# Kernel tuning notes

Measured on AMD Instinct MI355X. Metric: run time of the kernel, lower is better.

Reference implementation:

```python
import jax, jax.numpy as jnp
import numpy as np

B, D, T, C = 128, 128, 2048, 64


def setup_inputs() -> dict:
    key = jax.random.key(0)
    k1, k2, k3 = jax.random.split(key, 3)
    feature = jax.random.normal(k1, (B, D, T), dtype=jnp.float32)
    label = jax.random.randint(k2, (B, T), 0, C, dtype=jnp.int64)
    centers = jax.random.normal(k3, (C, D), dtype=jnp.float32)
    return {"feature": feature, "label": label, "centers": centers}


def reference(feature, label, centers):
    # feature: [B, D, T] -> flatten to [N, D] with N = B*T (transpose(2,1).reshape)
    num_classes, feat_dim = centers.shape
    feat = jnp.transpose(feature, (0, 2, 1)).reshape(-1, feat_dim)  # [N, D]
    lab = label.reshape(-1)                                          # [N]

    centers_batch = centers[lab]                                     # gather [N, D]
    center_loss = jnp.mean((feat - centers_batch) ** 2)              # MSELoss (mean)

    diff = centers_batch - feat                                      # [N, D]
    # scatter-sum of per-row diffs into their class slot (replaces python loop)
    difference = jax.ops.segment_sum(diff, lab, num_segments=num_classes)  # [C, D]
    appear_times = jnp.bincount(lab, length=num_classes)             # [C]
    difference = difference / jnp.clip(appear_times, 1, None).astype(difference.dtype)[:, None]
    return (center_loss, difference)
```

## Files before the change

kernel.cpp:

```cpp
#include <hip/hip_runtime.h>


#define NT 2048
#define NC 64

#define OFF_P     0
#define OFF_SSP   1048576
#define OFF_CNTP  1048832
#define OFF_CROSS 1057024
#define OFF_CC    1057056
#define OFF_SS    1057088

#define WAIT_VM0()   __builtin_amdgcn_s_waitcnt(0x0F70)
#define WAIT_VM4()   __builtin_amdgcn_s_waitcnt(0x0F74)
#define WAIT_LGKM0() __builtin_amdgcn_s_waitcnt(0xC07F)
#define CFENCE()     __asm__ volatile("" ::: "memory")
#define BAR()        do { CFENCE(); __builtin_amdgcn_s_barrier(); CFENCE(); } while (0)

__device__ __forceinline__ void dma16(const float* g, float* l) {
    __builtin_amdgcn_global_load_lds(
        (const __attribute__((address_space(1))) void*)g,
        (__attribute__((address_space(3))) void*)l, 16, 0, 0);
}

__global__ __launch_bounds__(256) void k_main(const float* __restrict__ feat,
                                              const int*  __restrict__ label,
                                              float* __restrict__ ws) {
    __shared__ float rowbuf[2][2][2052];
    __shared__ unsigned short __attribute__((aligned(16))) sorted[4096];
    __shared__ float S_lds[64][33];
    __shared__ float partial[2][256];
    __shared__ int cnt[NC], pstart[NC], ntc[NC], cursor[NC];

    const int tid = threadIdx.x, bid = blockIdx.x;
    const int dh = bid & 1, b = bid >> 1;
    const int wave = tid >> 6, lane = tid & 63;

    for (int j = tid; j < 4096; j += 256) sorted[j] = (unsigned short)8192;
    if (tid < NC) { cnt[tid] = 0; cursor[tid] = 0; }
    if (tid < 4) rowbuf[tid >> 1][tid & 1][2048] = 0.0f;
    __syncthreads();

    const int* lp = label + b * NT + tid * 8;
    const int4 La = *(const int4*)lp;
    const int4 Lb = *(const int4*)(lp + 4);
    atomicAdd(&cnt[La.x], 1); atomicAdd(&cnt[La.y], 1);
    atomicAdd(&cnt[La.z], 1); atomicAdd(&cnt[La.w], 1);
    atomicAdd(&cnt[Lb.x], 1); atomicAdd(&cnt[Lb.y], 1);
    atomicAdd(&cnt[Lb.z], 1); atomicAdd(&cnt[Lb.w], 1);
    __syncthreads();

    if (tid == 0) {
        int pt = 0;
        for (int c = 0; c < NC; ++c) {
            int pl = (cnt[c] + 15) & ~15;
            pstart[c] = pt; ntc[c] = pl >> 4; pt += pl;
        }
    }
    __syncthreads();

    if (dh == 0 && tid < NC) ((int*)(ws + OFF_CNTP))[b * NC + tid] = cnt[tid];

    {
        const int t0 = tid * 8;
        int l, p;
        l = La.x; p = pstart[l] + atomicAdd(&cursor[l], 1); sorted[p] = (unsigned short)((t0 + 0) * 4);
        l = La.y; p = pstart[l] + atomicAdd(&cursor[l], 1); sorted[p] = (unsigned short)((t0 + 1) * 4);
        l = La.z; p = pstart[l] + atomicAdd(&cursor[l], 1); sorted[p] = (unsigned short)((t0 + 2) * 4);
        l = La.w; p = pstart[l] + atomicAdd(&cursor[l], 1); sorted[p] = (unsigned short)((t0 + 3) * 4);
        l = Lb.x; p = pstart[l] + atomicAdd(&cursor[l], 1); sorted[p] = (unsigned short)((t0 + 4) * 4);
        l = Lb.y; p = pstart[l] + atomicAdd(&cursor[l], 1); sorted[p] = (unsigned short)((t0 + 5) * 4);
        l = Lb.z; p = pstart[l] + atomicAdd(&cursor[l], 1); sorted[p] = (unsigned short)((t0 + 6) * 4);
        l = Lb.w; p = pstart[l] + atomicAdd(&cursor[l], 1); sorted[p] = (unsigned short)((t0 + 7) * 4);
    }
    __syncthreads();

    int off[16];
    {
        const uint4 pk0 = *(const uint4*)&sorted[tid * 16];
        const uint4 pk1 = *(const uint4*)&sorted[tid * 16 + 8];
        off[0]  = pk0.x & 0xFFFF; off[1]  = pk0.x >> 16;
        off[2]  = pk0.y & 0xFFFF; off[3]  = pk0.y >> 16;
        off[4]  = pk0.z & 0xFFFF; off[5]  = pk0.z >> 16;
        off[6]  = pk0.w & 0xFFFF; off[7]  = pk0.w >> 16;
        off[8]  = pk1.x & 0xFFFF; off[9]  = pk1.x >> 16;
        off[10] = pk1.y & 0xFFFF; off[11] = pk1.y >> 16;
        off[12] = pk1.z & 0xFFFF; off[13] = pk1.z >> 16;
        off[14] = pk1.w & 0xFFFF; off[15] = pk1.w >> 16;
    }

    const float* fbase = feat + ((size_t)b * 128 + dh * 64) * NT;
    float ss = 0.0f;

    {
        #pragma unroll
        for (int q = 0; q < 4; ++q) {
            int m = wave + 4 * q, r = m >> 3, p = m & 7;
            dma16(fbase + (size_t)r * NT + p * 256 + lane * 4, &rowbuf[0][r][p * 256]);
        }
    }

    for (int i = 0; i < 32; ++i) {
        const int buf = i & 1;
        if (i < 31) {
            const float* base = fbase + (size_t)(2 * (i + 1)) * NT;
            #pragma unroll
            for (int q = 0; q < 4; ++q) {
                int m = wave + 4 * q, r = m >> 3, p = m & 7;
                dma16(base + (size_t)r * NT + p * 256 + lane * 4, &rowbuf[buf ^ 1][r][p * 256]);
            }
            WAIT_VM4();
        } else {
            WAIT_VM0();
        }
        BAR();

        #pragma unroll
        for (int r = 0; r < 2; ++r) {
            const char* rb = (const char*)&rowbuf[buf][r][0];
            float s = 0.0f;
            #pragma unroll
            for (int j = 0; j < 16; ++j) {
                float v = *(const float*)(rb + off[j]);
                s += v; ss += v * v;
            }
            partial[r][tid] = s;
        }
        WAIT_LGKM0();
        BAR();

        if (tid < 128) {
            const int c = tid & 63, r = tid >> 6;
            const int ft = pstart[c] >> 4, n = ntc[c];
            float s = 0.0f;
            for (int j = 0; j < n; ++j) s += partial[r][ft + j];
            S_lds[c][(2 * i + r) & 31] = s;
        }

        if ((i & 15) == 15) {
            WAIT_LGKM0();
            BAR();
            const int dbase = (i >> 4) << 5;
            const int c = tid >> 2, dj0 = (tid & 3) * 8;
            float4 v0, v1;
            v0.x = S_lds[c][dj0 + 0]; v0.y = S_lds[c][dj0 + 1];
            v0.z = S_lds[c][dj0 + 2]; v0.w = S_lds[c][dj0 + 3];
            v1.x = S_lds[c][dj0 + 4]; v1.y = S_lds[c][dj0 + 5];
            v1.z = S_lds[c][dj0 + 6]; v1.w = S_lds[c][dj0 + 7];
            float* dst = ws + OFF_P + (size_t)bid * 4096 + c * 64 + dbase + dj0;
            *(float4*)dst = v0;
            *(float4*)(dst + 4) = v1;
        }
    }

    __syncthreads();
    partial[0][tid] = ss;
    __syncthreads();
    for (int s = 128; s > 0; s >>= 1) {
        if (tid < s) partial[0][tid] += partial[0][tid + s];
        __syncthreads();
    }
    if (tid == 0) ws[OFF_SSP + bid] = partial[0][0];
}

__global__ __launch_bounds__(256) void k_red(float* __restrict__ ws,
                                             const float* __restrict__ centers,
                                             float* __restrict__ out) {
    const int tid = threadIdx.x, bid = blockIdx.x;

    if (bid == 32) {
        __shared__ float r[256];
        r[tid] = ws[OFF_SSP + tid];
        __syncthreads();
        for (int k = 128; k > 0; k >>= 1) { if (tid < k) r[tid] += r[tid + k]; __syncthreads(); }
        if (tid == 0) ws[OFF_SS] = r[0];
        return;
    }

    __shared__ int cred[256];
    __shared__ int cnt[NC];
    {
        const int c = tid & 63, part = tid >> 6;
        const int* cntP = (const int*)(ws + OFF_CNTP);
        int s = 0;
        for (int bb = part * 32; bb < part * 32 + 32; ++bb) s += cntP[bb * NC + c];
        cred[tid] = s;
    }
    __syncthreads();
    if (tid < NC) cnt[tid] = cred[tid] + cred[tid + 64] + cred[tid + 128] + cred[tid + 192];
    __syncthreads();

    const int e = bid * 256 + tid;
    const int c = e >> 7, d = e & 127, dhh = d >> 6, dl = d & 63;
    const float* Pp = ws + OFF_P + (size_t)dhh * 4096 + c * 64 + dl;
    float sum = 0.0f;
    #pragma unroll 8
    for (int bb = 0; bb < 128; ++bb) sum += Pp[(size_t)bb * 8192];

    const float ctr = centers[e];
    const float cn  = (float)cnt[c];
    const float den = cn > 1.0f ? cn : 1.0f;
    out[1 + e] = (cn * ctr - sum) / den;

    __shared__ float r1[256], r2[256];
    r1[tid] = sum * ctr;
    r2[tid] = cn * ctr * ctr;
    __syncthreads();
    for (int k = 128; k > 0; k >>= 1) {
        if (tid < k) { r1[tid] += r1[tid + k]; r2[tid] += r2[tid + k]; }
        __syncthreads();
    }
    if (tid == 0) { ws[OFF_CROSS + bid] = r1[0]; ws[OFF_CC + bid] = r2[0]; }
}

__global__ __launch_bounds__(64) void k_epi(const float* __restrict__ ws,
                                            float* __restrict__ out) {
    int t = threadIdx.x;
    float cr = (t < 32) ? ws[OFF_CROSS + t] : 0.0f;
    float cc = (t < 32) ? ws[OFF_CC + t] : 0.0f;
    for (int o = 16; o > 0; o >>= 1) { cr += __shfl_down(cr, o); cc += __shfl_down(cc, o); }
    if (t == 0) out[0] = (ws[OFF_SS] - 2.0f * cr + cc) * (1.0f / 33554432.0f);
}

extern "C" void kernel_launch(void* const* d_in, const int* in_sizes, int n_in,
                              void* d_out, int out_size, void* d_ws, size_t ws_size,
                              hipStream_t stream) {
    const float* feat    = (const float*)d_in[0];
    const int*   label   = (const int*)d_in[1];
    const float* centers = (const float*)d_in[2];
    float* out = (float*)d_out;
    float* ws  = (float*)d_ws;

    hipLaunchKernelGGL(k_main, dim3(256), dim3(256), 0, stream, feat, label, ws);
    hipLaunchKernelGGL(k_red,  dim3(33),  dim3(256), 0, stream, ws, centers, out);
    hipLaunchKernelGGL(k_epi,  dim3(1),   dim3(64),  0, stream, ws, out);
}
```

Before: 212.4 us.

## Split each batch's time axis across two blocks and overlap first load with sorting

Each batch/feature-half is now handled by two blocks, one per half of the time axis, so k_main launches 512 blocks. Each block does four feature rows per step over 1024 timesteps. The first feature DMA is issued before label counting and sorting, so that setup overlaps the load. The serial prefix sum over class counts becomes a wavefront shuffle scan. The reduction kernel now sums twice as many partial slices, which means more workspace traffic in exchange for more parallelism and occupancy in the main pass.

```diff
diff --git a/kernel.cpp b/kernel.cpp
--- a/kernel.cpp
+++ b/kernel.cpp
@@ -5,11 +5,11 @@
 #define NC 64
 
 #define OFF_P     0
-#define OFF_SSP   1048576
-#define OFF_CNTP  1048832
-#define OFF_CROSS 1057024
-#define OFF_CC    1057056
-#define OFF_SS    1057088
+#define OFF_SSP   2097152
+#define OFF_CNTP  2097664
+#define OFF_CROSS 2114048
+#define OFF_CC    2114080
+#define OFF_SS    2114112
 
 #define WAIT_VM0()   __builtin_amdgcn_s_waitcnt(0x0F70)
 #define WAIT_VM4()   __builtin_amdgcn_s_waitcnt(0x0F74)
@@ -26,89 +26,79 @@
 __global__ __launch_bounds__(256) void k_main(const float* __restrict__ feat,
                                               const int*  __restrict__ label,
                                               float* __restrict__ ws) {
-    __shared__ float rowbuf[2][2][2052];
-    __shared__ unsigned short __attribute__((aligned(16))) sorted[4096];
+    __shared__ float rowbuf[2][4][1028];
+    __shared__ unsigned short __attribute__((aligned(16))) sorted[2048];
     __shared__ float S_lds[64][33];
-    __shared__ float partial[2][256];
+    __shared__ float partial[4][256];
     __shared__ int cnt[NC], pstart[NC], ntc[NC], cursor[NC];
 
     const int tid = threadIdx.x, bid = blockIdx.x;
-    const int dh = bid & 1, b = bid >> 1;
+    const int th = bid & 1, dh = (bid >> 1) & 1, b = bid >> 2;
     const int wave = tid >> 6, lane = tid & 63;
 
-    for (int j = tid; j < 4096; j += 256) sorted[j] = (unsigned short)8192;
+    const float* fbase = feat + ((size_t)(b * 128 + dh * 64)) * NT + th * 1024;
+
+    #pragma unroll
+    for (int q = 0; q < 4; ++q)
+        dma16(fbase + (size_t)wave * NT + q * 256 + lane * 4, &rowbuf[0][wave][q * 256]);
+
+    for (int j = tid; j < 2048; j += 256) sorted[j] = (unsigned short)4096;
     if (tid < NC) { cnt[tid] = 0; cursor[tid] = 0; }
-    if (tid < 4) rowbuf[tid >> 1][tid & 1][2048] = 0.0f;
-    __syncthreads();
-
-    const int* lp = label + b * NT + tid * 8;
-    const int4 La = *(const int4*)lp;
-    const int4 Lb = *(const int4*)(lp + 4);
-    atomicAdd(&cnt[La.x], 1); atomicAdd(&cnt[La.y], 1);
-    atomicAdd(&cnt[La.z], 1); atomicAdd(&cnt[La.w], 1);
-    atomicAdd(&cnt[Lb.x], 1); atomicAdd(&cnt[Lb.y], 1);
-    atomicAdd(&cnt[Lb.z], 1); atomicAdd(&cnt[Lb.w], 1);
-    __syncthreads();
-
-    if (tid == 0) {
-        int pt = 0;
-        for (int c = 0; c < NC; ++c) {
-            int pl = (cnt[c] + 15) & ~15;
-            pstart[c] = pt; ntc[c] = pl >> 4; pt += pl;
-        }
-    }
-    __syncthreads();
-
-    if (dh == 0 && tid < NC) ((int*)(ws + OFF_CNTP))[b * NC + tid] = cnt[tid];
+    if (tid < 8) rowbuf[tid >> 2][tid & 3][1024] = 0.0f;
+    __syncthreads();
+
+    const int* lp = label + b * NT + th * 1024 + tid * 4;
+    const int4 L = *(const int4*)lp;
+    atomicAdd(&cnt[L.x], 1); atomicAdd(&cnt[L.y], 1);
+    atomicAdd(&cnt[L.z], 1); atomicAdd(&cnt[L.w], 1);
+    __syncthreads();
+
+    if (tid < 64) {
+        const int pl = (cnt[tid] + 7) & ~7;
+        int incl = pl;
+        #pragma unroll
+        for (int o = 1; o < 64; o <<= 1) {
+            int n = __shfl_up(incl, o);
+            if (tid >= o) incl += n;
+        }
+        pstart[tid] = incl - pl;
+        ntc[tid]    = pl >> 3;
+    }
+    __syncthreads();
+
+    if (dh == 0 && tid < NC) ((int*)(ws + OFF_CNTP))[(b * 2 + th) * NC + tid] = cnt[tid];
 
     {
-        const int t0 = tid * 8;
+        const int t0 = tid * 4;
         int l, p;
-        l = La.x; p = pstart[l] + atomicAdd(&cursor[l], 1); sorted[p] = (unsigned short)((t0 + 0) * 4);
-        l = La.y; p = pstart[l] + atomicAdd(&cursor[l], 1); sorted[p] = (unsigned short)((t0 + 1) * 4);
-        l = La.z; p = pstart[l] + atomicAdd(&cursor[l], 1); sorted[p] = (unsigned short)((t0 + 2) * 4);
-        l = La.w; p = pstart[l] + atomicAdd(&cursor[l], 1); sorted[p] = (unsigned short)((t0 + 3) * 4);
-        l = Lb.x; p = pstart[l] + atomicAdd(&cursor[l], 1); sorted[p] = (unsigned short)((t0 + 4) * 4);
-        l = Lb.y; p = pstart[l] + atomicAdd(&cursor[l], 1); sorted[p] = (unsigned short)((t0 + 5) * 4);
-        l = Lb.z; p = pstart[l] + atomicAdd(&cursor[l], 1); sorted[p] = (unsigned short)((t0 + 6) * 4);
-        l = Lb.w; p = pstart[l] + atomicAdd(&cursor[l], 1); sorted[p] = (unsigned short)((t0 + 7) * 4);
-    }
-    __syncthreads();
-
-    int off[16];
+        l = L.x; p = pstart[l] + atomicAdd(&cursor[l], 1); sorted[p] = (unsigned short)((t0 + 0) * 4);
+        l = L.y; p = pstart[l] + atomicAdd(&cursor[l], 1); sorted[p] = (unsigned short)((t0 + 1) * 4);
+        l = L.z; p = pstart[l] + atomicAdd(&cursor[l], 1); sorted[p] = (unsigned short)((t0 + 2) * 4);
+        l = L.w; p = pstart[l] + atomicAdd(&cursor[l], 1); sorted[p] = (unsigned short)((t0 + 3) * 4);
+    }
+    __syncthreads();
+
+    int off[8];
     {
-        const uint4 pk0 = *(const uint4*)&sorted[tid * 16];
-        const uint4 pk1 = *(const uint4*)&sorted[tid * 16 + 8];
-        off[0]  = pk0.x & 0xFFFF; off[1]  = pk0.x >> 16;
-        off[2]  = pk0.y & 0xFFFF; off[3]  = pk0.y >> 16;
-        off[4]  = pk0.z & 0xFFFF; off[5]  = pk0.z >> 16;
-        off[6]  = pk0.w & 0xFFFF; off[7]  = pk0.w >> 16;
-        off[8]  = pk1.x & 0xFFFF; off[9]  = pk1.x >> 16;
-        off[10] = pk1.y & 0xFFFF; off[11] = pk1.y >> 16;
-        off[12] = pk1.z & 0xFFFF; off[13] = pk1.z >> 16;
-        off[14] = pk1.w & 0xFFFF; off[15] = pk1.w >> 16;
-    }
-
-    const float* fbase = feat + ((size_t)b * 128 + dh * 64) * NT;
+        const uint4 pk = *(const uint4*)&sorted[tid * 8];
+        off[0] = pk.x & 0xFFFF; off[1] = pk.x >> 16;
+        off[2] = pk.y & 0xFFFF; off[3] = pk.y >> 16;
+        off[4] = pk.z & 0xFFFF; off[5] = pk.z >> 16;
+        off[6] = pk.w & 0xFFFF; off[7] = pk.w >> 16;
+    }
+
+    const int oc = tid & 63, orow = tid >> 6;
+    const int ft = pstart[oc] >> 3, on = ntc[oc];
+
     float ss = 0.0f;
 
-    {
-        #pragma unroll
-        for (int q = 0; q < 4; ++q) {
-            int m = wave + 4 * q, r = m >> 3, p = m & 7;
-            dma16(fbase + (size_t)r * NT + p * 256 + lane * 4, &rowbuf[0][r][p * 256]);
-        }
-    }
-
-    for (int i = 0; i < 32; ++i) {
+    for (int i = 0; i < 16; ++i) {
         const int buf = i & 1;
-        if (i < 31) {
-            const float* base = fbase + (size_t)(2 * (i + 1)) * NT;
+        if (i < 15) {
+            const float* base = fbase + (size_t)(4 * (i + 1) + wave) * NT;
             #pragma unroll
-            for (int q = 0; q < 4; ++q) {
-                int m = wave + 4 * q, r = m >> 3, p = m & 7;
-                dma16(base + (size_t)r * NT + p * 256 + lane * 4, &rowbuf[buf ^ 1][r][p * 256]);
-            }
+            for (int q = 0; q < 4; ++q)
+                dma16(base + q * 256 + lane * 4, &rowbuf[buf ^ 1][wave][q * 256]);
             WAIT_VM4();
         } else {
             WAIT_VM0();
@@ -116,11 +106,11 @@
         BAR();
 
         #pragma unroll
-        for (int r = 0; r < 2; ++r) {
+        for (int r = 0; r < 4; ++r) {
             const char* rb = (const char*)&rowbuf[buf][r][0];
             float s = 0.0f;
             #pragma unroll
-            for (int j = 0; j < 16; ++j) {
+            for (int j = 0; j < 8; ++j) {
                 float v = *(const float*)(rb + off[j]);
                 s += v; ss += v * v;
             }
@@ -129,18 +119,16 @@
         WAIT_LGKM0();
         BAR();
 
-        if (tid < 128) {
-            const int c = tid & 63, r = tid >> 6;
-            const int ft = pstart[c] >> 4, n = ntc[c];
+        {
             float s = 0.0f;
-            for (int j = 0; j < n; ++j) s += partial[r][ft + j];
-            S_lds[c][(2 * i + r) & 31] = s;
-        }
-
-        if ((i & 15) == 15) {
+            for (int j = 0; j < on; ++j) s += partial[orow][ft + j];
+            S_lds[oc][(4 * i + orow) & 31] = s;
+        }
+
+        if ((i & 7) == 7) {
             WAIT_LGKM0();
             BAR();
-            const int dbase = (i >> 4) << 5;
+            const int dbase = (i >> 3) << 5;
             const int c = tid >> 2, dj0 = (tid & 3) * 8;
             float4 v0, v1;
             v0.x = S_lds[c][dj0 + 0]; v0.y = S_lds[c][dj0 + 1];
@@ -170,7 +158,7 @@
 
     if (bid == 32) {
         __shared__ float r[256];
-        r[tid] = ws[OFF_SSP + tid];
+        r[tid] = ws[OFF_SSP + tid] + ws[OFF_SSP + 256 + tid];
         __syncthreads();
         for (int k = 128; k > 0; k >>= 1) { if (tid < k) r[tid] += r[tid + k]; __syncthreads(); }
         if (tid == 0) ws[OFF_SS] = r[0];
@@ -183,7 +171,7 @@
         const int c = tid & 63, part = tid >> 6;
         const int* cntP = (const int*)(ws + OFF_CNTP);
         int s = 0;
-        for (int bb = part * 32; bb < part * 32 + 32; ++bb) s += cntP[bb * NC + c];
+        for (int e2 = part * 64; e2 < part * 64 + 64; ++e2) s += cntP[e2 * NC + c];
         cred[tid] = s;
     }
     __syncthreads();
@@ -192,10 +180,11 @@
 
     const int e = bid * 256 + tid;
     const int c = e >> 7, d = e & 127, dhh = d >> 6, dl = d & 63;
-    const float* Pp = ws + OFF_P + (size_t)dhh * 4096 + c * 64 + dl;
+    const float* Pp = ws + OFF_P + (size_t)(dhh * 2) * 4096 + c * 64 + dl;
     float sum = 0.0f;
     #pragma unroll 8
-    for (int bb = 0; bb < 128; ++bb) sum += Pp[(size_t)bb * 8192];
+    for (int bb = 0; bb < 128; ++bb)
+        sum += Pp[(size_t)bb * 16384] + Pp[(size_t)bb * 16384 + 4096];
 
     const float ctr = centers[e];
     const float cn  = (float)cnt[c];
@@ -231,7 +220,7 @@
     float* out = (float*)d_out;
     float* ws  = (float*)d_ws;
 
-    hipLaunchKernelGGL(k_main, dim3(256), dim3(256), 0, stream, feat, label, ws);
+    hipLaunchKernelGGL(k_main, dim3(512), dim3(256), 0, stream, feat, label, ws);
     hipLaunchKernelGGL(k_red,  dim3(33),  dim3(256), 0, stream, ws, centers, out);
     hipLaunchKernelGGL(k_epi,  dim3(1),   dim3(64),  0, stream, ws, out);
 }
```

Measured after the change: 219.6 us. 1.03x slower.
